# Performance work log

Measured on AMD Instinct MI355X. Metric: run time of the kernel, lower is better.

## Reference

```python
import jax, jax.numpy as jnp
import numpy as np

N = 4096
NFEAT = 256
NHID1 = 64
NHID2 = 32
NCLASS = 8
NHEADS = 4
NADJ = 2
ALPHA = 0.2  # leaky relu slope
NEG = -9e15


def setup_inputs() -> dict:
    key = jax.random.key(0)
    ks = jax.random.split(key, 14)
    x = jax.random.normal(ks[0], (N, NFEAT), jnp.float32)
    adj = (jax.random.uniform(ks[1], (NADJ, N, N)) < 0.01).astype(jnp.float32)
    adj = jnp.maximum(adj, jnp.eye(N, dtype=jnp.float32)[None])
    s = 0.05
    W1 = jax.random.normal(ks[2], (NADJ, NHEADS, NFEAT, NHID1), jnp.float32) * s
    a1 = jax.random.normal(ks[3], (NADJ, NHEADS, 2, NHID1), jnp.float32) * s
    W2 = jax.random.normal(ks[4], (NADJ, NHEADS, NHID1, NHID2), jnp.float32) * s
    a2 = jax.random.normal(ks[5], (NADJ, NHEADS, 2, NHID2), jnp.float32) * s
    Wi1 = jax.random.normal(ks[6], (NHID1 * NHEADS, NHID1), jnp.float32) * s
    bi1 = jnp.zeros((NHID1,), jnp.float32)
    Wi2 = jax.random.normal(ks[7], (NHID2 * NHEADS, NCLASS), jnp.float32) * s
    bi2 = jnp.zeros((NCLASS,), jnp.float32)
    Wf = jax.random.normal(ks[8], (NCLASS * NADJ, NCLASS), jnp.float32) * s
    bf = jnp.zeros((NCLASS,), jnp.float32)
    return {"x": x, "adj": adj, "W1": W1, "a1": a1, "W2": W2, "a2": a2,
            "Wi1": Wi1, "bi1": bi1, "Wi2": Wi2, "bi2": bi2, "Wf": Wf, "bf": bf}


def gat_multihead(x, adj_i, W, a):
    # x: [n, f]; adj_i: [n, n]; W: [h, f, o]; a: [h, 2, o]
    Wh = jnp.einsum('nf,hfo->hno', x, W)                 # [h, n, o]
    f_src = jnp.einsum('hno,ho->hn', Wh, a[:, 0])        # [h, n]
    f_dst = jnp.einsum('hno,ho->hn', Wh, a[:, 1])        # [h, n]
    e = jax.nn.leaky_relu(f_src[:, :, None] + f_dst[:, None, :], ALPHA)
    e = jnp.where(adj_i[None] > 0, e, NEG)               # masked scores [h, n, n]
    att = jax.nn.softmax(e, axis=-1)
    h = jnp.einsum('hnm,hmo->hno', att, Wh)              # aggregate
    h = jax.nn.elu(h)                                     # concat=True -> elu
    n = x.shape[0]
    return jnp.transpose(h, (1, 0, 2)).reshape(n, -1)     # [n, h*o]


def reference(x, adj, W1, a1, W2, a2, Wi1, bi1, Wi2, bi2, Wf, bf):
    outs = []
    for i in range(NADJ):  # small fixed loop over adjacency graphs
        xi = gat_multihead(x, adj[i], W1[i], a1[i])
        xi = jax.nn.elu(xi @ Wi1 + bi1)
        xi = gat_multihead(xi, adj[i], W2[i], a2[i])
        xi = jax.nn.elu(xi @ Wi2 + bi2)
        outs.append(xi)
    out = jnp.concatenate(outs, axis=1) @ Wf + bf         # [n, nclass]
    l1_loss = jnp.mean(jnp.abs(Wf))
    return jax.nn.log_softmax(out, axis=1), l1_loss
```

## Files before the change

kernel.cpp:

```cpp
#include <hip/hip_runtime.h>
#include <hip/hip_bf16.h>

#define NN 4096
#define NFEAT 256
#define NHID1 64
#define NHID2 32
#define NCLASS 8
#define NHEADS 4
#define NADJ 2
#define CAP 128

__device__ __forceinline__ unsigned short f2bf(float v) {
  unsigned int x = __float_as_uint(v);
  return (unsigned short)((x + 0x7fffu + ((x >> 16) & 1u)) >> 16);
}

template <int KDIM, int NDIM, int RPTY, int ACT, int COEF, int OBF16>
__device__ __forceinline__ void gemm_body(
    const float* __restrict__ A, const float* __restrict__ B,
    const float* __restrict__ bias, void* __restrict__ C,
    const float* __restrict__ ag, float* __restrict__ fsrc,
    float* __restrict__ fdst, const int row0b,
    float* __restrict__ sA, float* __restrict__ sB) {
  constexpr int KT = 32;
  constexpr int TX = NDIM / 4;
  constexpr int TY = 256 / TX;
  constexpr int BR = TY * RPTY;
  constexpr int LDA = BR + 4;
  constexpr int LDB = NDIM + 4;
  const int tid = threadIdx.x;
  const int tx = tid % TX, ty = tid / TX;
  const int c0 = tx * 4;
  float acc[RPTY][4];
#pragma unroll
  for (int i = 0; i < RPTY; ++i)
#pragma unroll
    for (int j = 0; j < 4; ++j) acc[i][j] = 0.f;

  for (int kt = 0; kt < KDIM; kt += KT) {
    __syncthreads();
    for (int i = tid; i < BR * (KT / 4); i += 256) {
      const int r = i / (KT / 4), e = i % (KT / 4);
      const float4 v = *(const float4*)(A + (size_t)(row0b + r) * KDIM + kt + e * 4);
      sA[(e * 4 + 0) * LDA + r] = v.x;
      sA[(e * 4 + 1) * LDA + r] = v.y;
      sA[(e * 4 + 2) * LDA + r] = v.z;
      sA[(e * 4 + 3) * LDA + r] = v.w;
    }
    for (int i = tid; i < KT * (NDIM / 4); i += 256) {
      const int k = i / (NDIM / 4), cc = i % (NDIM / 4);
      *(float4*)&sB[k * LDB + cc * 4] = *(const float4*)(B + (size_t)(kt + k) * NDIM + cc * 4);
    }
    __syncthreads();
#pragma unroll
    for (int k = 0; k < KT; ++k) {
      float a4[RPTY];
      if constexpr (RPTY == 4) {
        const float4 t = *(const float4*)&sA[k * LDA + ty * 4];
        a4[0] = t.x; a4[1] = t.y; a4[2] = t.z; a4[3] = t.w;
      } else {
        const float2 t = *(const float2*)&sA[k * LDA + ty * 2];
        a4[0] = t.x; a4[1] = t.y;
      }
      const float4 bv = *(const float4*)&sB[k * LDB + c0];
      const float b4[4] = {bv.x, bv.y, bv.z, bv.w};
#pragma unroll
      for (int i = 0; i < RPTY; ++i)
#pragma unroll
        for (int j = 0; j < 4; ++j) acc[i][j] += a4[i] * b4[j];
    }
  }
  float b4[4] = {0.f, 0.f, 0.f, 0.f};
  if (bias) {
    const float4 bb = *(const float4*)&bias[c0];
    b4[0] = bb.x; b4[1] = bb.y; b4[2] = bb.z; b4[3] = bb.w;
  }
#pragma unroll
  for (int i = 0; i < RPTY; ++i) {
    const int row = row0b + ty * RPTY + i;
    float v[4];
#pragma unroll
    for (int j = 0; j < 4; ++j) {
      v[j] = acc[i][j] + b4[j];
      if (ACT == 1) v[j] = v[j] > 0.f ? v[j] : (__expf(v[j]) - 1.f);
    }
    if constexpr (OBF16) {
      ushort4 o;
      o.x = f2bf(v[0]); o.y = f2bf(v[1]); o.z = f2bf(v[2]); o.w = f2bf(v[3]);
      *(ushort4*)((unsigned short*)C + (size_t)row * NDIM + c0) = o;
    } else {
      float4 o;
      o.x = v[0]; o.y = v[1]; o.z = v[2]; o.w = v[3];
      *(float4*)((float*)C + (size_t)row * NDIM + c0) = o;
    }
  }
  if constexpr (COEF) {
    float aS[4], aD[4];
#pragma unroll
    for (int j = 0; j < 4; ++j) { aS[j] = ag[c0 + j]; aD[j] = ag[NDIM + c0 + j]; }
#pragma unroll
    for (int i = 0; i < RPTY; ++i) {
      float s = 0.f, d = 0.f;
#pragma unroll
      for (int j = 0; j < 4; ++j) { s += acc[i][j] * aS[j]; d += acc[i][j] * aD[j]; }
#pragma unroll
      for (int off = TX / 2; off; off >>= 1) {
        s += __shfl_xor(s, off);
        d += __shfl_xor(d, off);
      }
      if (tx == 0) {
        const int row = row0b + ty * RPTY + i;
        fsrc[row] = s;
        fdst[row] = d;
      }
    }
  }
}

__global__ __launch_bounds__(256) void k1_gemm_edges(
    const float* __restrict__ x, const float* __restrict__ W1,
    const float* __restrict__ a1, unsigned short* __restrict__ Wh1,
    float* __restrict__ fs1, float* __restrict__ fd1,
    const float* __restrict__ adj, int* __restrict__ eidx,
    int* __restrict__ ecnt) {
  __shared__ float sA[32 * (64 + 4)];
  __shared__ float sB[32 * (64 + 4)];
  constexpr int NB_GEMM = (NN / 64) * NHEADS * NADJ;
  if (blockIdx.x < NB_GEMM) {
    int b = blockIdx.x;
    const int tile = b % (NN / 64); b /= (NN / 64);
    const int h = b % NHEADS;
    const int g = b / NHEADS;
    const int gh = g * NHEADS + h;
    gemm_body<NFEAT, NHID1, 4, 0, 1, 1>(
        x, W1 + (size_t)gh * NFEAT * NHID1, nullptr,
        Wh1 + (size_t)gh * NN * NHID1, a1 + (size_t)gh * 2 * NHID1,
        fs1 + (size_t)gh * NN, fd1 + (size_t)gh * NN, tile * 64, sA, sB);
  } else {
    const int wave = threadIdx.x >> 6;
    const int lane = threadIdx.x & 63;
    const int r = (blockIdx.x - NB_GEMM) * 4 + wave;
    const float4* row = (const float4*)(adj + (size_t)r * NN);
    int* out = eidx + (size_t)r * CAP;
    int base = 0;
    for (int c = 0; c < NN; c += 256) {
      const float4 v = row[(c >> 2) + lane];
      const int j0 = c + lane * 4;
      const float vt[4] = {v.x, v.y, v.z, v.w};
#pragma unroll
      for (int t = 0; t < 4; ++t) {
        const bool hit = vt[t] > 0.f;
        const unsigned long long m = __ballot(hit);
        if (hit) {
          const int pos = base + __popcll(m & ((1ull << lane) - 1ull));
          if (pos < CAP) out[pos] = j0 + t;
        }
        base += __popcll(m);
      }
    }
    if (lane == 0) ecnt[r] = base < CAP ? base : CAP;
  }
}

template <int KDIM, int NDIM, int RPTY, int ACT, int COEF, int OBF16>
__global__ __launch_bounds__(256) void gemm_tile(
    const float* __restrict__ A, const float* __restrict__ B,
    const float* __restrict__ bias, void* __restrict__ C,
    const float* __restrict__ av, float* __restrict__ fsrc,
    float* __restrict__ fdst,
    size_t asG, size_t bsH, size_t bsG, size_t csH, size_t csG) {
  constexpr int TX = NDIM / 4;
  constexpr int TY = 256 / TX;
  constexpr int BR = TY * RPTY;
  __shared__ float sA[32 * (BR + 4)];
  __shared__ float sB[32 * (NDIM + 4)];
  const int g = blockIdx.z, h = blockIdx.y;
  const int gh = g * NHEADS + h;
  void* Cp;
  if constexpr (OBF16)
    Cp = (void*)((unsigned short*)C + (size_t)g * csG + (size_t)h * csH);
  else
    Cp = (void*)((float*)C + (size_t)g * csG + (size_t)h * csH);
  gemm_body<KDIM, NDIM, RPTY, ACT, COEF, OBF16>(
      A + (size_t)g * asG, B + (size_t)g * bsG + (size_t)h * bsH, bias, Cp,
      COEF ? av + (size_t)gh * 2 * NDIM : nullptr,
      COEF ? fsrc + (size_t)gh * NN : nullptr,
      COEF ? fdst + (size_t)gh * NN : nullptr,
      (int)blockIdx.x * BR, sA, sB);
}

#define GATB(ACC, JJ)                                                          \
  {                                                                            \
    const float w_ = wgt[wave][JJ];                                            \
    const uint4 v_ = *(const uint4*)(WhH + (size_t)midx[wave][JJ] * O + c8);   \
    ACC[0] += w_ * __uint_as_float(v_.x << 16);                                \
    ACC[1] += w_ * __uint_as_float(v_.x & 0xffff0000u);                        \
    ACC[2] += w_ * __uint_as_float(v_.y << 16);                                \
    ACC[3] += w_ * __uint_as_float(v_.y & 0xffff0000u);                        \
    ACC[4] += w_ * __uint_as_float(v_.z << 16);                                \
    ACC[5] += w_ * __uint_as_float(v_.z & 0xffff0000u);                        \
    ACC[6] += w_ * __uint_as_float(v_.w << 16);                                \
    ACC[7] += w_ * __uint_as_float(v_.w & 0xffff0000u);                        \
  }

template <int O>
__global__ __launch_bounds__(256) void aggregate(
    const unsigned short* __restrict__ Wh, const float* __restrict__ fsrc,
    const float* __restrict__ fdst, const int* __restrict__ eidx,
    const int* __restrict__ ecnt, float* __restrict__ Hout) {
  constexpr int CPL = O / 8;
  constexpr int EPW = 64 / CPL;
  __shared__ float wgt[4][CAP];
  __shared__ int midx[4][CAP];
  const int wave = threadIdx.x >> 6;
  const int lane = threadIdx.x & 63;
  const int n = blockIdx.x * 4 + wave;
  const int h = blockIdx.y, g = blockIdx.z;
  const int gh = g * NHEADS + h;
  const int cnt = ecnt[(size_t)g * NN + n];
  const int* ei = eidx + (size_t)(g * NN + n) * CAP;
  const float fs = fsrc[(size_t)gh * NN + n];
  const float* fd = fdst + (size_t)gh * NN;
  float mx = -3.4e38f;
  for (int j = lane; j < cnt; j += 64) {
    const int m = ei[j];
    float e = fs + fd[m];
    e = e > 0.f ? e : 0.2f * e;
    midx[wave][j] = m;
    wgt[wave][j] = e;
    mx = fmaxf(mx, e);
  }
  for (int off = 32; off; off >>= 1) mx = fmaxf(mx, __shfl_xor(mx, off));
  float sm = 0.f;
  for (int j = lane; j < cnt; j += 64) {
    const float w = __expf(wgt[wave][j] - mx);
    wgt[wave][j] = w;
    sm += w;
  }
  for (int off = 32; off; off >>= 1) sm += __shfl_xor(sm, off);
  const unsigned short* WhH = Wh + (size_t)gh * NN * O;
  const int sub = lane / CPL;
  const int c8 = (lane % CPL) * 8;
  float A0[8] = {0, 0, 0, 0, 0, 0, 0, 0};
  float A1[8] = {0, 0, 0, 0, 0, 0, 0, 0};
  int j = sub;
  for (; j + EPW < cnt; j += 2 * EPW) {
    GATB(A0, j);
    GATB(A1, j + EPW);
  }
  for (; j < cnt; j += EPW) GATB(A0, j);
#pragma unroll
  for (int q = 0; q < 8; ++q) A0[q] += A1[q];
#pragma unroll
  for (int off = CPL; off < 64; off <<= 1)
#pragma unroll
    for (int q = 0; q < 8; ++q) A0[q] += __shfl_xor(A0[q], off);
  if (lane < CPL) {
    const float inv = 1.f / sm;
    float o[8];
#pragma unroll
    for (int q = 0; q < 8; ++q) {
      o[q] = A0[q] * inv;
      o[q] = o[q] > 0.f ? o[q] : (__expf(o[q]) - 1.f);
    }
    float* dst = Hout + (size_t)g * NN * (NHEADS * O) + (size_t)n * (NHEADS * O) +
                 h * O + lane * 8;
    float4 o0, o1;
    o0.x = o[0]; o0.y = o[1]; o0.z = o[2]; o0.w = o[3];
    o1.x = o[4]; o1.y = o[5]; o1.z = o[6]; o1.w = o[7];
    *(float4*)dst = o0;
    *(float4*)(dst + 4) = o1;
  }
}

__global__ __launch_bounds__(256) void tail_fused(const float* __restrict__ h2,
                                                  const float* __restrict__ Wi2,
                                                  const float* __restrict__ bi2,
                                                  const float* __restrict__ Wf,
                                                  const float* __restrict__ bfv,
                                                  float* __restrict__ out) {
  constexpr int K = NHEADS * NHID2;
  __shared__ float A0[16][K + 4];
  __shared__ float A1[16][K + 4];
  __shared__ float Bs[K][NCLASS];
  __shared__ float WfS[2 * NCLASS][NCLASS];
  __shared__ float cat[16][2 * NCLASS + 1];
  const int tid = threadIdx.x;
  const int row0 = blockIdx.x * 16;
  for (int i = tid; i < 16 * (K / 4); i += 256) {
    const int r = i >> 5, e = i & 31;
    *(float4*)&A0[r][e * 4] = *(const float4*)(h2 + (size_t)(row0 + r) * K + e * 4);
    *(float4*)&A1[r][e * 4] =
        *(const float4*)(h2 + (size_t)NN * K + (size_t)(row0 + r) * K + e * 4);
  }
  ((float4*)Bs)[tid] = ((const float4*)Wi2)[tid];
  if (tid < 32) ((float4*)WfS)[tid] = ((const float4*)Wf)[tid];
  __syncthreads();
  const int c = tid & 7;
  const int kk = (tid >> 3) & 1;
  const int r = tid >> 4;
  float s0 = kk ? 0.f : bi2[c], s1 = kk ? 0.f : bi2[c];
#pragma unroll 8
  for (int k = kk * (K / 2); k < (kk + 1) * (K / 2); ++k) {
    s0 += A0[r][k] * Bs[k][c];
    s1 += A1[r][k] * Bs[k][c];
  }
  s0 += __shfl_xor(s0, 8);
  s1 += __shfl_xor(s1, 8);
  if (kk == 0) {
    cat[r][c] = s0 > 0.f ? s0 : (__expf(s0) - 1.f);
    cat[r][NCLASS + c] = s1 > 0.f ? s1 : (__expf(s1) - 1.f);
  }
  __syncthreads();
  float logit = bfv[c];
#pragma unroll
  for (int k = 0; k < 2 * NCLASS; ++k) logit += cat[r][k] * WfS[k][c];
  float m = logit;
#pragma unroll
  for (int off = 4; off; off >>= 1) m = fmaxf(m, __shfl_xor(m, off));
  float s = __expf(logit - m);
#pragma unroll
  for (int off = 4; off; off >>= 1) s += __shfl_xor(s, off);
  if (kk == 0) out[(size_t)(row0 + r) * NCLASS + c] = logit - (logf(s) + m);
  if (blockIdx.x == 0 && tid < 64) {
    float v = fabsf(Wf[tid]) + fabsf(Wf[64 + tid]);
    for (int off = 32; off; off >>= 1) v += __shfl_xor(v, off);
    if (tid == 0) out[NN * NCLASS] = v * (1.f / (2 * NCLASS * NCLASS));
  }
}

extern "C" void kernel_launch(void* const* d_in, const int* in_sizes, int n_in,
                              void* d_out, int out_size, void* d_ws, size_t ws_size,
                              hipStream_t stream) {
  const float* x = (const float*)d_in[0];
  const float* adj = (const float*)d_in[1];
  const float* W1 = (const float*)d_in[2];
  const float* a1 = (const float*)d_in[3];
  const float* W2 = (const float*)d_in[4];
  const float* a2 = (const float*)d_in[5];
  const float* Wi1 = (const float*)d_in[6];
  const float* bi1 = (const float*)d_in[7];
  const float* Wi2 = (const float*)d_in[8];
  const float* bi2 = (const float*)d_in[9];
  const float* Wf = (const float*)d_in[10];
  const float* bfv = (const float*)d_in[11];
  float* out = (float*)d_out;

  char* ws = (char*)d_ws;
  int* eidx = (int*)ws;            ws += (size_t)NADJ * NN * CAP * 4;
  int* ecnt = (int*)ws;            ws += (size_t)NADJ * NN * 4;
  unsigned short* Wh1 = (unsigned short*)ws;
  ws += (size_t)NADJ * NHEADS * NN * NHID1 * 2;
  float* fs1 = (float*)ws;         ws += (size_t)NADJ * NHEADS * NN * 4;
  float* fd1 = (float*)ws;         ws += (size_t)NADJ * NHEADS * NN * 4;
  float* h1 = (float*)ws;          ws += (size_t)NADJ * NN * NHEADS * NHID1 * 4;
  float* x1 = (float*)ws;          ws += (size_t)NADJ * NN * NHID1 * 4;
  unsigned short* Wh2 = (unsigned short*)ws;
  ws += (size_t)NADJ * NHEADS * NN * NHID2 * 2;
  float* fs2 = (float*)ws;         ws += (size_t)NADJ * NHEADS * NN * 4;
  float* fd2 = (float*)ws;         ws += (size_t)NADJ * NHEADS * NN * 4;
  float* h2 = (float*)ws;          ws += (size_t)NADJ * NN * NHEADS * NHID2 * 4;

  k1_gemm_edges<<<512 + NADJ * NN / 4, 256, 0, stream>>>(
      x, W1, a1, Wh1, fs1, fd1, adj, eidx, ecnt);

  aggregate<NHID1><<<dim3(NN / 4, NHEADS, NADJ), 256, 0, stream>>>(
      Wh1, fs1, fd1, eidx, ecnt, h1);

  gemm_tile<NHEADS * NHID1, NHID1, 2, 1, 0, 0><<<dim3(NN / 32, 1, NADJ), 256, 0, stream>>>(
      h1, Wi1, bi1, x1, nullptr, nullptr, nullptr,
      (size_t)NN * NHEADS * NHID1, 0, 0, 0, (size_t)NN * NHID1);

  gemm_tile<NHID1, NHID2, 4, 0, 1, 1><<<dim3(NN / 128, NHEADS, NADJ), 256, 0, stream>>>(
      x1, W2, nullptr, Wh2, a2, fs2, fd2,
      (size_t)NN * NHID1, (size_t)NHID1 * NHID2, (size_t)NHEADS * NHID1 * NHID2,
      (size_t)NN * NHID2, (size_t)NHEADS * NN * NHID2);

  aggregate<NHID2><<<dim3(NN / 4, NHEADS, NADJ), 256, 0, stream>>>(
      Wh2, fs2, fd2, eidx, ecnt, h2);

  tail_fused<<<NN / 16, 256, 0, stream>>>(h2, Wi2, bi2, Wf, bfv, out);
}
```

Before: 101.0 us.

## Fuse inter-layer GEMMs and fuse second aggregation with tail

Merges the Wi1 projection (with bias and ELU) and the per-head W2 projection plus attention coefficients into one kernel, keeping x1 in shared memory instead of writing it to global memory. The second-layer aggregation is also fused with the Wi2/Wf/log-softmax tail in a 512-thread kernel that handles two rows across both graphs and all heads, removing the h2 buffer. This cuts six launches to four and drops intermediate global round trips. The trade-offs are lower parallelism per block and a scalar inner loop for the W2 GEMM.

New measurement: 110.6 us. +9.5%, slower.

```diff
diff --git a/kernel.cpp b/kernel.cpp
--- a/kernel.cpp
+++ b/kernel.cpp
@@ -15,12 +15,11 @@
   return (unsigned short)((x + 0x7fffu + ((x >> 16) & 1u)) >> 16);
 }
 
-template <int KDIM, int NDIM, int RPTY, int ACT, int COEF, int OBF16>
+template <int KDIM, int NDIM, int RPTY>
 __device__ __forceinline__ void gemm_body(
     const float* __restrict__ A, const float* __restrict__ B,
-    const float* __restrict__ bias, void* __restrict__ C,
-    const float* __restrict__ ag, float* __restrict__ fsrc,
-    float* __restrict__ fdst, const int row0b,
+    unsigned short* __restrict__ C, const float* __restrict__ ag,
+    float* __restrict__ fsrc, float* __restrict__ fdst, const int row0b,
     float* __restrict__ sA, float* __restrict__ sB) {
   constexpr int KT = 32;
   constexpr int TX = NDIM / 4;
@@ -54,14 +53,8 @@
     __syncthreads();
 #pragma unroll
     for (int k = 0; k < KT; ++k) {
-      float a4[RPTY];
-      if constexpr (RPTY == 4) {
-        const float4 t = *(const float4*)&sA[k * LDA + ty * 4];
-        a4[0] = t.x; a4[1] = t.y; a4[2] = t.z; a4[3] = t.w;
-      } else {
-        const float2 t = *(const float2*)&sA[k * LDA + ty * 2];
-        a4[0] = t.x; a4[1] = t.y;
-      }
+      const float4 t = *(const float4*)&sA[k * LDA + ty * 4];
+      const float a4[4] = {t.x, t.y, t.z, t.w};
       const float4 bv = *(const float4*)&sB[k * LDB + c0];
       const float b4[4] = {bv.x, bv.y, bv.z, bv.w};
 #pragma unroll
@@ -70,49 +63,31 @@
         for (int j = 0; j < 4; ++j) acc[i][j] += a4[i] * b4[j];
     }
   }
-  float b4[4] = {0.f, 0.f, 0.f, 0.f};
-  if (bias) {
-    const float4 bb = *(const float4*)&bias[c0];
-    b4[0] = bb.x; b4[1] = bb.y; b4[2] = bb.z; b4[3] = bb.w;
-  }
 #pragma unroll
   for (int i = 0; i < RPTY; ++i) {
     const int row = row0b + ty * RPTY + i;
-    float v[4];
-#pragma unroll
-    for (int j = 0; j < 4; ++j) {
-      v[j] = acc[i][j] + b4[j];
-      if (ACT == 1) v[j] = v[j] > 0.f ? v[j] : (__expf(v[j]) - 1.f);
-    }
-    if constexpr (OBF16) {
-      ushort4 o;
-      o.x = f2bf(v[0]); o.y = f2bf(v[1]); o.z = f2bf(v[2]); o.w = f2bf(v[3]);
-      *(ushort4*)((unsigned short*)C + (size_t)row * NDIM + c0) = o;
-    } else {
-      float4 o;
-      o.x = v[0]; o.y = v[1]; o.z = v[2]; o.w = v[3];
-      *(float4*)((float*)C + (size_t)row * NDIM + c0) = o;
-    }
-  }
-  if constexpr (COEF) {
-    float aS[4], aD[4];
-#pragma unroll
-    for (int j = 0; j < 4; ++j) { aS[j] = ag[c0 + j]; aD[j] = ag[NDIM + c0 + j]; }
-#pragma unroll
-    for (int i = 0; i < RPTY; ++i) {
-      float s = 0.f, d = 0.f;
-#pragma unroll
-      for (int j = 0; j < 4; ++j) { s += acc[i][j] * aS[j]; d += acc[i][j] * aD[j]; }
-#pragma unroll
-      for (int off = TX / 2; off; off >>= 1) {
-        s += __shfl_xor(s, off);
-        d += __shfl_xor(d, off);
-      }
-      if (tx == 0) {
-        const int row = row0b + ty * RPTY + i;
-        fsrc[row] = s;
-        fdst[row] = d;
-      }
+    ushort4 o;
+    o.x = f2bf(acc[i][0]); o.y = f2bf(acc[i][1]);
+    o.z = f2bf(acc[i][2]); o.w = f2bf(acc[i][3]);
+    *(ushort4*)(C + (size_t)row * NDIM + c0) = o;
+  }
+  float aS[4], aD[4];
+#pragma unroll
+  for (int j = 0; j < 4; ++j) { aS[j] = ag[c0 + j]; aD[j] = ag[NDIM + c0 + j]; }
+#pragma unroll
+  for (int i = 0; i < RPTY; ++i) {
+    float s = 0.f, d = 0.f;
+#pragma unroll
+    for (int j = 0; j < 4; ++j) { s += acc[i][j] * aS[j]; d += acc[i][j] * aD[j]; }
+#pragma unroll
+    for (int off = TX / 2; off; off >>= 1) {
+      s += __shfl_xor(s, off);
+      d += __shfl_xor(d, off);
+    }
+    if (tx == 0) {
+      const int row = row0b + ty * RPTY + i;
+      fsrc[row] = s;
+      fdst[row] = d;
     }
   }
 }
@@ -132,10 +107,10 @@
     const int h = b % NHEADS;
     const int g = b / NHEADS;
     const int gh = g * NHEADS + h;
-    gemm_body<NFEAT, NHID1, 4, 0, 1, 1>(
-        x, W1 + (size_t)gh * NFEAT * NHID1, nullptr,
-        Wh1 + (size_t)gh * NN * NHID1, a1 + (size_t)gh * 2 * NHID1,
-        fs1 + (size_t)gh * NN, fd1 + (size_t)gh * NN, tile * 64, sA, sB);
+    gemm_body<NFEAT, NHID1, 4>(
+        x, W1 + (size_t)gh * NFEAT * NHID1, Wh1 + (size_t)gh * NN * NHID1,
+        a1 + (size_t)gh * 2 * NHID1, fs1 + (size_t)gh * NN,
+        fd1 + (size_t)gh * NN, tile * 64, sA, sB);
   } else {
     const int wave = threadIdx.x >> 6;
     const int lane = threadIdx.x & 63;
@@ -162,37 +137,10 @@
   }
 }
 
-template <int KDIM, int NDIM, int RPTY, int ACT, int COEF, int OBF16>
-__global__ __launch_bounds__(256) void gemm_tile(
-    const float* __restrict__ A, const float* __restrict__ B,
-    const float* __restrict__ bias, void* __restrict__ C,
-    const float* __restrict__ av, float* __restrict__ fsrc,
-    float* __restrict__ fdst,
-    size_t asG, size_t bsH, size_t bsG, size_t csH, size_t csG) {
-  constexpr int TX = NDIM / 4;
-  constexpr int TY = 256 / TX;
-  constexpr int BR = TY * RPTY;
-  __shared__ float sA[32 * (BR + 4)];
-  __shared__ float sB[32 * (NDIM + 4)];
-  const int g = blockIdx.z, h = blockIdx.y;
-  const int gh = g * NHEADS + h;
-  void* Cp;
-  if constexpr (OBF16)
-    Cp = (void*)((unsigned short*)C + (size_t)g * csG + (size_t)h * csH);
-  else
-    Cp = (void*)((float*)C + (size_t)g * csG + (size_t)h * csH);
-  gemm_body<KDIM, NDIM, RPTY, ACT, COEF, OBF16>(
-      A + (size_t)g * asG, B + (size_t)g * bsG + (size_t)h * bsH, bias, Cp,
-      COEF ? av + (size_t)gh * 2 * NDIM : nullptr,
-      COEF ? fsrc + (size_t)gh * NN : nullptr,
-      COEF ? fdst + (size_t)gh * NN : nullptr,
-      (int)blockIdx.x * BR, sA, sB);
-}
-
-#define GATB(ACC, JJ)                                                          \
+#define GATB(ACC, JJ, OO)                                                      \
   {                                                                            \
     const float w_ = wgt[wave][JJ];                                            \
-    const uint4 v_ = *(const uint4*)(WhH + (size_t)midx[wave][JJ] * O + c8);   \
+    const uint4 v_ = *(const uint4*)(WhH + (size_t)midx[wave][JJ] * OO + c8);  \
     ACC[0] += w_ * __uint_as_float(v_.x << 16);                                \
     ACC[1] += w_ * __uint_as_float(v_.x & 0xffff0000u);                        \
     ACC[2] += w_ * __uint_as_float(v_.y << 16);                                \
@@ -203,11 +151,11 @@
     ACC[7] += w_ * __uint_as_float(v_.w & 0xffff0000u);                        \
   }
 
-template <int O>
-__global__ __launch_bounds__(256) void aggregate(
+__global__ __launch_bounds__(256) void aggregate1(
     const unsigned short* __restrict__ Wh, const float* __restrict__ fsrc,
     const float* __restrict__ fdst, const int* __restrict__ eidx,
     const int* __restrict__ ecnt, float* __restrict__ Hout) {
+  constexpr int O = NHID1;
   constexpr int CPL = O / 8;
   constexpr int EPW = 64 / CPL;
   __shared__ float wgt[4][CAP];
@@ -245,10 +193,10 @@
   float A1[8] = {0, 0, 0, 0, 0, 0, 0, 0};
   int j = sub;
   for (; j + EPW < cnt; j += 2 * EPW) {
-    GATB(A0, j);
-    GATB(A1, j + EPW);
-  }
-  for (; j < cnt; j += EPW) GATB(A0, j);
+    GATB(A0, j, O);
+    GATB(A1, j + EPW, O);
+  }
+  for (; j < cnt; j += EPW) GATB(A0, j, O);
 #pragma unroll
   for (int q = 0; q < 8; ++q) A0[q] += A1[q];
 #pragma unroll
@@ -273,59 +221,253 @@
   }
 }
 
-__global__ __launch_bounds__(256) void tail_fused(const float* __restrict__ h2,
-                                                  const float* __restrict__ Wi2,
-                                                  const float* __restrict__ bi2,
-                                                  const float* __restrict__ Wf,
-                                                  const float* __restrict__ bfv,
-                                                  float* __restrict__ out) {
-  constexpr int K = NHEADS * NHID2;
-  __shared__ float A0[16][K + 4];
-  __shared__ float A1[16][K + 4];
-  __shared__ float Bs[K][NCLASS];
-  __shared__ float WfS[2 * NCLASS][NCLASS];
-  __shared__ float cat[16][2 * NCLASS + 1];
+__global__ __launch_bounds__(256) void k3_inter_gemm2(
+    const float* __restrict__ h1, const float* __restrict__ Wi1,
+    const float* __restrict__ bi1, const float* __restrict__ W2,
+    const float* __restrict__ a2, unsigned short* __restrict__ Wh2,
+    float* __restrict__ fs2, float* __restrict__ fd2) {
+  __shared__ float sA[32 * 36];
+  __shared__ float sB[32 * 68];
+  __shared__ float x1s[32 * 68];
+  __shared__ float W2s[NHEADS * 64 * 32];
+  const int g = blockIdx.y;
+  const int n0 = blockIdx.x * 32;
   const int tid = threadIdx.x;
-  const int row0 = blockIdx.x * 16;
-  for (int i = tid; i < 16 * (K / 4); i += 256) {
-    const int r = i >> 5, e = i & 31;
-    *(float4*)&A0[r][e * 4] = *(const float4*)(h2 + (size_t)(row0 + r) * K + e * 4);
-    *(float4*)&A1[r][e * 4] =
-        *(const float4*)(h2 + (size_t)NN * K + (size_t)(row0 + r) * K + e * 4);
-  }
-  ((float4*)Bs)[tid] = ((const float4*)Wi2)[tid];
+  const float* A = h1 + (size_t)g * NN * (NHEADS * NHID1);
+
+  const int tx = tid & 15, ty = tid >> 4;
+  const int c0 = tx * 4;
+  float acc[2][4] = {{0.f, 0.f, 0.f, 0.f}, {0.f, 0.f, 0.f, 0.f}};
+  for (int kt = 0; kt < 256; kt += 32) {
+    __syncthreads();
+    for (int i = tid; i < 32 * 8; i += 256) {
+      const int r = i >> 3, e = i & 7;
+      const float4 v = *(const float4*)(A + (size_t)(n0 + r) * 256 + kt + e * 4);
+      sA[(e * 4 + 0) * 36 + r] = v.x;
+      sA[(e * 4 + 1) * 36 + r] = v.y;
+      sA[(e * 4 + 2) * 36 + r] = v.z;
+      sA[(e * 4 + 3) * 36 + r] = v.w;
+    }
+    for (int i = tid; i < 32 * 16; i += 256) {
+      const int k = i >> 4, cc = i & 15;
+      *(float4*)&sB[k * 68 + cc * 4] = *(const float4*)(Wi1 + (size_t)(kt + k) * 64 + cc * 4);
+    }
+    __syncthreads();
+#pragma unroll
+    for (int k = 0; k < 32; ++k) {
+      const float2 t = *(const float2*)&sA[k * 36 + ty * 2];
+      const float4 bv = *(const float4*)&sB[k * 68 + c0];
+      const float b4[4] = {bv.x, bv.y, bv.z, bv.w};
+#pragma unroll
+      for (int j = 0; j < 4; ++j) {
+        acc[0][j] += t.x * b4[j];
+        acc[1][j] += t.y * b4[j];
+      }
+    }
+  }
+  {
+    const float4 bb = *(const float4*)&bi1[c0];
+    const float b4[4] = {bb.x, bb.y, bb.z, bb.w};
+#pragma unroll
+    for (int i = 0; i < 2; ++i) {
+      float4 o;
+      float* op = (float*)&o;
+#pragma unroll
+      for (int j = 0; j < 4; ++j) {
+        float v = acc[i][j] + b4[j];
+        op[j] = v > 0.f ? v : (__expf(v) - 1.f);
+      }
+      *(float4*)&x1s[(ty * 2 + i) * 68 + c0] = o;
+    }
+  }
+  {
+    const float4* w2p = (const float4*)(W2 + (size_t)g * NHEADS * NHID1 * NHID2);
+    for (int i = tid; i < 2048; i += 256) ((float4*)W2s)[i] = w2p[i];
+  }
+  __syncthreads();
+
+  const int c = tid & 31, rg = tid >> 5;
+  for (int h = 0; h < NHEADS; ++h) {
+    const int gh = g * NHEADS + h;
+    float a4[4] = {0.f, 0.f, 0.f, 0.f};
+    for (int k = 0; k < 64; ++k) {
+      const float w = W2s[(h * 64 + k) * 32 + c];
+#pragma unroll
+      for (int i = 0; i < 4; ++i) a4[i] += x1s[(rg * 4 + i) * 68 + k] * w;
+    }
+    const float* ag = a2 + (size_t)gh * 2 * NHID2;
+    const float aS = ag[c], aD = ag[NHID2 + c];
+#pragma unroll
+    for (int i = 0; i < 4; ++i) {
+      const int row = n0 + rg * 4 + i;
+      Wh2[((size_t)gh * NN + row) * NHID2 + c] = f2bf(a4[i]);
+      float s = a4[i] * aS, d = a4[i] * aD;
+#pragma unroll
+      for (int off = 16; off; off >>= 1) {
+        s += __shfl_xor(s, off);
+        d += __shfl_xor(d, off);
+      }
+      if (c == 0) {
+        fs2[(size_t)gh * NN + row] = s;
+        fd2[(size_t)gh * NN + row] = d;
+      }
+    }
+  }
+}
+
+__global__ __launch_bounds__(512) void k4_agg2_tail(
+    const unsigned short* __restrict__ Wh2, const float* __restrict__ fs2,
+    const float* __restrict__ fd2, const int* __restrict__ eidx,
+    const int* __restrict__ ecnt, const float* __restrict__ Wi2,
+    const float* __restrict__ bi2, const float* __restrict__ Wf,
+    const float* __restrict__ bfv, float* __restrict__ out) {
+  constexpr int O = NHID2;
+  __shared__ float Wi2s[128 * 8];
+  __shared__ float WfS[16 * 8];
+  __shared__ float h2cat[2][260];
+  __shared__ float cat[2][17];
+  __shared__ float wgt[8][CAP];
+  __shared__ int midx[2][2][CAP];
+  const int n0 = blockIdx.x * 2;
+  const int tid = threadIdx.x;
+  const int wave = tid >> 6;
+  const int lane = tid & 63;
+
+  for (int i = tid; i < 256; i += 512) ((float4*)Wi2s)[i] = ((const float4*)Wi2)[i];
   if (tid < 32) ((float4*)WfS)[tid] = ((const float4*)Wf)[tid];
+  for (int i = tid; i < 4 * CAP; i += 512) {
+    const int g_ = i >> 8, rr = (i >> 7) & 1, j = i & (CAP - 1);
+    midx[g_][rr][j] = eidx[(size_t)(g_ * NN + n0 + rr) * CAP + j];
+  }
   __syncthreads();
-  const int c = tid & 7;
-  const int kk = (tid >> 3) & 1;
-  const int r = tid >> 4;
-  float s0 = kk ? 0.f : bi2[c], s1 = kk ? 0.f : bi2[c];
-#pragma unroll 8
-  for (int k = kk * (K / 2); k < (kk + 1) * (K / 2); ++k) {
-    s0 += A0[r][k] * Bs[k][c];
-    s1 += A1[r][k] * Bs[k][c];
-  }
-  s0 += __shfl_xor(s0, 8);
-  s1 += __shfl_xor(s1, 8);
-  if (kk == 0) {
-    cat[r][c] = s0 > 0.f ? s0 : (__expf(s0) - 1.f);
-    cat[r][NCLASS + c] = s1 > 0.f ? s1 : (__expf(s1) - 1.f);
+
+  const int g = wave >> 2, h = wave & 3;
+  const int gh = g * NHEADS + h;
+  const unsigned short* WhH = Wh2 + (size_t)gh * NN * O;
+  const float* fdv = fd2 + (size_t)gh * NN;
+  for (int rr = 0; rr < 2; ++rr) {
+    const int n = n0 + rr;
+    const int cnt = ecnt[g * NN + n];
+    const float fsv = fs2[(size_t)gh * NN + n];
+    float mx = -3.4e38f;
+    for (int j = lane; j < cnt; j += 64) {
+      float e = fsv + fdv[midx[g][rr][j]];
+      e = e > 0.f ? e : 0.2f * e;
+      wgt[wave][j] = e;
+      mx = fmaxf(mx, e);
+    }
+    for (int off = 32; off; off >>= 1) mx = fmaxf(mx, __shfl_xor(mx, off));
+    float sm = 0.f;
+    for (int j = lane; j < cnt; j += 64) {
+      const float w = __expf(wgt[wave][j] - mx);
+      wgt[wave][j] = w;
+      sm += w;
+    }
+    for (int off = 32; off; off >>= 1) sm += __shfl_xor(sm, off);
+    const int sub = lane >> 2;
+    const int c8 = (lane & 3) * 8;
+    float A0[8] = {0, 0, 0, 0, 0, 0, 0, 0};
+    float A1[8] = {0, 0, 0, 0, 0, 0, 0, 0};
+    {
+      const int wv = wave;
+      const int* mi = midx[g][rr];
+      int j = sub;
+      for (; j + 16 < cnt; j += 32) {
+        {
+          const float w_ = wgt[wv][j];
+          const uint4 v_ = *(const uint4*)(WhH + (size_t)mi[j] * O + c8);
+          A0[0] += w_ * __uint_as_float(v_.x << 16);
+          A0[1] += w_ * __uint_as_float(v_.x & 0xffff0000u);
+          A0[2] += w_ * __uint_as_float(v_.y << 16);
+          A0[3] += w_ * __uint_as_float(v_.y & 0xffff0000u);
+          A0[4] += w_ * __uint_as_float(v_.z << 16);
+          A0[5] += w_ * __uint_as_float(v_.z & 0xffff0000u);
+          A0[6] += w_ * __uint_as_float(v_.w << 16);
+          A0[7] += w_ * __uint_as_float(v_.w & 0xffff0000u);
+        }
+        {
+          const float w_ = wgt[wv][j + 16];
+          const uint4 v_ = *(const uint4*)(WhH + (size_t)mi[j + 16] * O + c8);
+          A1[0] += w_ * __uint_as_float(v_.x << 16);
+          A1[1] += w_ * __uint_as_float(v_.x & 0xffff0000u);
+          A1[2] += w_ * __uint_as_float(v_.y << 16);
+          A1[3] += w_ * __uint_as_float(v_.y & 0xffff0000u);
+          A1[4] += w_ * __uint_as_float(v_.z << 16);
+          A1[5] += w_ * __uint_as_float(v_.z & 0xffff0000u);
+          A1[6] += w_ * __uint_as_float(v_.w << 16);
+          A1[7] += w_ * __uint_as_float(v_.w & 0xffff0000u);
+        }
+      }
+      for (; j < cnt; j += 16) {
+        const float w_ = wgt[wv][j];
+        const uint4 v_ = *(const uint4*)(WhH + (size_t)mi[j] * O + c8);
+        A0[0] += w_ * __uint_as_float(v_.x << 16);
+        A0[1] += w_ * __uint_as_float(v_.x & 0xffff0000u);
+        A0[2] += w_ * __uint_as_float(v_.y << 16);
+        A0[3] += w_ * __uint_as_float(v_.y & 0xffff0000u);
+        A0[4] += w_ * __uint_as_float(v_.z << 16);
+        A0[5] += w_ * __uint_as_float(v_.z & 0xffff0000u);
+        A0[6] += w_ * __uint_as_float(v_.w << 16);
+        A0[7] += w_ * __uint_as_float(v_.w & 0xffff0000u);
+      }
+    }
+#pragma unroll
+    for (int q = 0; q < 8; ++q) A0[q] += A1[q];
+#pragma unroll
+    for (int off = 4; off < 64; off <<= 1)
+#pragma unroll
+      for (int q = 0; q < 8; ++q) A0[q] += __shfl_xor(A0[q], off);
+    if (lane < 4) {
+      const float inv = 1.f / sm;
+      float o[8];
+#pragma unroll
+      for (int q = 0; q < 8; ++q) {
+        o[q] = A0[q] * inv;
+        o[q] = o[q] > 0.f ? o[q] : (__expf(o[q]) - 1.f);
+      }
+      float4 o0, o1;
+      o0.x = o[0]; o0.y = o[1]; o0.z = o[2]; o0.w = o[3];
+      o1.x = o[4]; o1.y = o[5]; o1.z = o[6]; o1.w = o[7];
+      float* dst = &h2cat[rr][g * 128 + h * O + (lane & 3) * 8];
+      *(float4*)dst = o0;
+      *(float4*)(dst + 4) = o1;
+    }
   }
   __syncthreads();
-  float logit = bfv[c];
-#pragma unroll
-  for (int k = 0; k < 2 * NCLASS; ++k) logit += cat[r][k] * WfS[k][c];
-  float m = logit;
-#pragma unroll
-  for (int off = 4; off; off >>= 1) m = fmaxf(m, __shfl_xor(m, off));
-  float s = __expf(logit - m);
-#pragma unroll
-  for (int off = 4; off; off >>= 1) s += __shfl_xor(s, off);
-  if (kk == 0) out[(size_t)(row0 + r) * NCLASS + c] = logit - (logf(s) + m);
-  if (blockIdx.x == 0 && tid < 64) {
-    float v = fabsf(Wf[tid]) + fabsf(Wf[64 + tid]);
+
+  {
+    const int r = tid >> 8, gg = (tid >> 7) & 1, c = (tid >> 4) & 7, kc = tid & 15;
+    float s = 0.f;
+#pragma unroll
+    for (int k = kc * 8; k < kc * 8 + 8; ++k)
+      s += h2cat[r][gg * 128 + k] * Wi2s[k * 8 + c];
+#pragma unroll
+    for (int off = 8; off; off >>= 1) s += __shfl_xor(s, off);
+    if (kc == 0) {
+      const float v = s + bi2[c];
+      cat[r][gg * 8 + c] = v > 0.f ? v : (__expf(v) - 1.f);
+    }
+  }
+  __syncthreads();
+
+  if (tid < 16) {
+    const int r = tid >> 3, c = tid & 7;
+    float logit = bfv[c];
+#pragma unroll
+    for (int k = 0; k < 16; ++k) logit += cat[r][k] * WfS[k * 8 + c];
+    float m = logit;
+#pragma unroll
+    for (int off = 4; off; off >>= 1) m = fmaxf(m, __shfl_xor(m, off));
+    float s = __expf(logit - m);
+#pragma unroll
+    for (int off = 4; off; off >>= 1) s += __shfl_xor(s, off);
+    out[(size_t)(n0 + r) * NCLASS + c] = logit - (logf(s) + m);
+  }
+  if (blockIdx.x == 0 && tid >= 64 && tid < 128) {
+    const int t = tid - 64;
+    float v = fabsf(Wf[t]) + fabsf(Wf[64 + t]);
     for (int off = 32; off; off >>= 1) v += __shfl_xor(v, off);
-    if (tid == 0) out[NN * NCLASS] = v * (1.f / (2 * NCLASS * NCLASS));
+    if (t == 0) out[NN * NCLASS] = v * (1.f / (2 * NCLASS * NCLASS));
   }
 }
 
@@ -354,30 +496,20 @@
   float* fs1 = (float*)ws;         ws += (size_t)NADJ * NHEADS * NN * 4;
   float* fd1 = (float*)ws;         ws += (size_t)NADJ * NHEADS * NN * 4;
   float* h1 = (float*)ws;          ws += (size_t)NADJ * NN * NHEADS * NHID1 * 4;
-  float* x1 = (float*)ws;          ws += (size_t)NADJ * NN * NHID1 * 4;
   unsigned short* Wh2 = (unsigned short*)ws;
   ws += (size_t)NADJ * NHEADS * NN * NHID2 * 2;
   float* fs2 = (float*)ws;         ws += (size_t)NADJ * NHEADS * NN * 4;
   float* fd2 = (float*)ws;         ws += (size_t)NADJ * NHEADS * NN * 4;
-  float* h2 = (float*)ws;          ws += (size_t)NADJ * NN * NHEADS * NHID2 * 4;
 
   k1_gemm_edges<<<512 + NADJ * NN / 4, 256, 0, stream>>>(
       x, W1, a1, Wh1, fs1, fd1, adj, eidx, ecnt);
 
-  aggregate<NHID1><<<dim3(NN / 4, NHEADS, NADJ), 256, 0, stream>>>(
+  aggregate1<<<dim3(NN / 4, NHEADS, NADJ), 256, 0, stream>>>(
       Wh1, fs1, fd1, eidx, ecnt, h1);
 
-  gemm_tile<NHEADS * NHID1, NHID1, 2, 1, 0, 0><<<dim3(NN / 32, 1, NADJ), 256, 0, stream>>>(
-      h1, Wi1, bi1, x1, nullptr, nullptr, nullptr,
-      (size_t)NN * NHEADS * NHID1, 0, 0, 0, (size_t)NN * NHID1);
-
-  gemm_tile<NHID1, NHID2, 4, 0, 1, 1><<<dim3(NN / 128, NHEADS, NADJ), 256, 0, stream>>>(
-      x1, W2, nullptr, Wh2, a2, fs2, fd2,
-      (size_t)NN * NHID1, (size_t)NHID1 * NHID2, (size_t)NHEADS * NHID1 * NHID2,
-      (size_t)NN * NHID2, (size_t)NHEADS * NN * NHID2);
-
-  aggregate<NHID2><<<dim3(NN / 4, NHEADS, NADJ), 256, 0, stream>>>(
-      Wh2, fs2, fd2, eidx, ecnt, h2);
-
-  tail_fused<<<NN / 16, 256, 0, stream>>>(h2, Wi2, bi2, Wf, bfv, out);
-}
+  k3_inter_gemm2<<<dim3(NN / 32, NADJ), 256, 0, stream>>>(
+      h1, Wi1, bi1, W2, a2, Wh2, fs2, fd2);
+
+  k4_agg2_tail<<<NN / 2, 512, 0, stream>>>(
+      Wh2, fs2, fd2, eidx, ecnt, Wi2, bi2, Wf, bfv, out);
+}
```
